# Kernel optimization log

Hardware: AMD Instinct MI355X
Metric: run time of the kernel (lower is better)

## Reference

```python
import jax, jax.numpy as jnp
import numpy as np
import math

B, H, S, D = 2, 8, 2048, 64

def setup_inputs() -> dict:
    key = jax.random.key(0)
    kq, kk, kv, km = jax.random.split(key, 4)
    query = jax.random.uniform(kq, (B, H, S, D), dtype=jnp.float32)
    key_t = jax.random.uniform(kk, (B, H, S, D), dtype=jnp.float32)
    value = jax.random.normal(kv, (B, H, S, D), dtype=jnp.float32)
    mask = jax.random.randint(km, (B, 1, 1, S), 0, 2, dtype=jnp.int32)
    return {"query": query, "key": key_t, "value": value, "mask": mask}

def reference(query, key, value, mask):
    # Non-standard: exp() applied to raw QK^T logits, THEN divided by sqrt(d)
    scores = jnp.exp(jnp.einsum('bhqd,bhkd->bhqk', query, key)) / math.sqrt(query.shape[-1])
    scores = jnp.where(mask == 0, jnp.float32(-1e9), scores)
    p_attn = jax.nn.softmax(scores, axis=-1)
    out = jnp.einsum('bhqk,bhkd->bhqd', p_attn, value)
    return (out, p_attn)
```

## Files before the change

kernel.cpp:

```cpp
#include <hip/hip_runtime.h>
#include <hip/hip_bf16.h>
#include <math.h>

#define NB 2
#define NH 8
#define NS 2048
#define ND 64
#define NBH (NB*NH)
#define QB 128
#define KT 64
#define NTILES (NS/KT)
#define NTHR 512
#define KSTR 72

typedef short bf16x8 __attribute__((ext_vector_type(8)));
typedef short bf16x4 __attribute__((ext_vector_type(4)));
typedef float f32x16 __attribute__((ext_vector_type(16)));

__device__ __forceinline__ short f2bf_trunc(float x){
  unsigned u = __builtin_bit_cast(unsigned, x);
  return (short)(u >> 16);
}
__device__ __forceinline__ float bf2f(short s){
  unsigned u = ((unsigned)(unsigned short)s) << 16;
  return __builtin_bit_cast(float, u);
}
__device__ __forceinline__ short f2bf_rn(float x){
  unsigned u = __builtin_bit_cast(unsigned, x);
  unsigned r = u + 0x7FFFu + ((u >> 16) & 1u);
  return (short)(r >> 16);
}
__device__ __forceinline__ void split3(float x, short &h, short &m, short &lo){
  h = f2bf_trunc(x);  float fh = bf2f(h);
  float r1 = x - fh;  m = f2bf_trunc(r1); float fm = bf2f(m);
  float r2 = r1 - fm; lo = f2bf_trunc(r2);
}

__global__ __launch_bounds__(NTHR, 2)
void attn_mfma_kernel(const float* __restrict__ Qg, const float* __restrict__ Kg,
                      const float* __restrict__ Vg, const int* __restrict__ Mg,
                      float* __restrict__ outO, float* __restrict__ outP)
{
  __shared__ __align__(16) short sKh[KT*KSTR];
  __shared__ __align__(16) short sKm[KT*KSTR];
  __shared__ __align__(16) short sKl[KT*KSTR];
  __shared__ __align__(16) short sVT[ND*KSTR];
  __shared__ __align__(16) short sP[QB*KSTR];
  __shared__ unsigned sMaskW[NS/32];
  __shared__ float sRedM[8*32], sRedS[8*32];

  const int tid = threadIdx.x;
  const int w  = tid >> 6;
  const int l  = tid & 63;
  const int wm = w >> 1;
  const int wn = w & 1;
  const int lc = l & 31;
  const int lh = l >> 5;

  const int bh = blockIdx.x >> 4;
  const int q0 = (blockIdx.x & 15) * QB;
  const int bb = bh >> 3;
  const size_t base = (size_t)bh * NS * ND;

  if (tid < NS/32) {
    unsigned wbits = 0;
    const int* mp = Mg + bb*NS + tid*32;
    #pragma unroll
    for (int i = 0; i < 32; ++i) wbits |= (mp[i] ? (1u << i) : 0u);
    sMaskW[tid] = wbits;
  }

  bf16x8 qh[4], qm[4], ql[4];
  {
    const float* qp = Qg + base + (size_t)(q0 + wm*32 + lc) * ND;
    #pragma unroll
    for (int ks = 0; ks < 4; ++ks) {
      const int d0 = ks*16 + lh*8;
      float4 f0 = *(const float4*)(qp + d0);
      float4 f1 = *(const float4*)(qp + d0 + 4);
      float xs[8] = {f0.x,f0.y,f0.z,f0.w,f1.x,f1.y,f1.z,f1.w};
      #pragma unroll
      for (int j = 0; j < 8; ++j) {
        short h, m, lo; split3(xs[j], h, m, lo);
        qh[ks][j] = h; qm[ks][j] = m; ql[ks][j] = lo;
      }
    }
  }

  const int s_kk = tid >> 3;
  const int s_d8 = (tid & 7) * 8;
  float4 ka, kb;
  auto loadK = [&](int kt){
    const float* kp = Kg + base + (size_t)(kt*KT + s_kk)*ND + s_d8;
    ka = *(const float4*)(kp);
    kb = *(const float4*)(kp + 4);
  };
  auto writeK = [&](){
    float xs[8] = {ka.x,ka.y,ka.z,ka.w,kb.x,kb.y,kb.z,kb.w};
    bf16x8 vh, vm, vl;
    #pragma unroll
    for (int j = 0; j < 8; ++j) {
      short h, m, lo; split3(xs[j], h, m, lo);
      vh[j] = h; vm[j] = m; vl[j] = lo;
    }
    const int off = s_kk*KSTR + s_d8;
    *(bf16x8*)(&sKh[off]) = vh;
    *(bf16x8*)(&sKm[off]) = vm;
    *(bf16x8*)(&sKl[off]) = vl;
  };

  const int v_dd = tid & 63;
  const int v_k4 = (tid >> 6) * 4;
  float va[4], vb[4];
  auto loadV = [&](int kt){
    const float* vp = Vg + base + (size_t)(kt*KT)*ND + v_dd;
    #pragma unroll
    for (int i = 0; i < 4; ++i) {
      va[i] = vp[(v_k4 + i) * ND];
      vb[i] = vp[(v_k4 + 32 + i) * ND];
    }
  };
  auto writeV = [&](){
    const int swz = ((v_dd >> 3) & 7) << 3;
    bf16x4 pa, pb;
    #pragma unroll
    for (int i = 0; i < 4; ++i) { pa[i] = f2bf_rn(va[i]); pb[i] = f2bf_rn(vb[i]); }
    *(bf16x4*)(&sVT[v_dd*KSTR + (v_k4 ^ swz)])        = pa;
    *(bf16x4*)(&sVT[v_dd*KSTR + ((v_k4 + 32) ^ swz)]) = pb;
  };

  auto qk_tile = [&](f32x16 &accA, f32x16 &accB){
    #pragma unroll
    for (int ks = 0; ks < 4; ++ks) {
      const int off = (wn*32 + lc)*KSTR + ks*16 + lh*8;
      bf16x8 b_h = *(const bf16x8*)(&sKh[off]);
      bf16x8 b_m = *(const bf16x8*)(&sKm[off]);
      bf16x8 b_l = *(const bf16x8*)(&sKl[off]);
      accA = __builtin_amdgcn_mfma_f32_32x32x16_bf16(qh[ks], b_h, accA, 0, 0, 0);
      accB = __builtin_amdgcn_mfma_f32_32x32x16_bf16(qh[ks], b_m, accB, 0, 0, 0);
      accB = __builtin_amdgcn_mfma_f32_32x32x16_bf16(qm[ks], b_h, accB, 0, 0, 0);
      accB = __builtin_amdgcn_mfma_f32_32x32x16_bf16(qm[ks], b_m, accB, 0, 0, 0);
      accB = __builtin_amdgcn_mfma_f32_32x32x16_bf16(qh[ks], b_l, accB, 0, 0, 0);
      accB = __builtin_amdgcn_mfma_f32_32x32x16_bf16(ql[ks], b_h, accB, 0, 0, 0);
    }
  };

  float mx[16], sm[16];
  #pragma unroll
  for (int r = 0; r < 16; ++r) { mx[r] = -INFINITY; sm[r] = 0.f; }

  loadK(0);
  #pragma unroll 1
  for (int kt = 0; kt < NTILES; ++kt) {
    writeK();
    __syncthreads();
    if (kt + 1 < NTILES) loadK(kt + 1);

    f32x16 accA, accB;
    #pragma unroll
    for (int r = 0; r < 16; ++r) { accA[r] = 0.f; accB[r] = 0.f; }
    qk_tile(accA, accB);

    const unsigned mbit = (sMaskW[kt*2 + wn] >> lc) & 1u;
    #pragma unroll
    for (int r = 0; r < 16; ++r) {
      float qk = accA[r] + accB[r];
      float s  = mbit ? __expf(qk) * 0.125f : -1e9f;
      float d  = s - mx[r];
      float e  = __expf(-__builtin_fabsf(d));
      bool  gt = d > 0.f;
      sm[r] = gt ? __builtin_fmaf(sm[r], e, 1.f) : (sm[r] + e);
      mx[r] = gt ? s : mx[r];
    }
    __syncthreads();
  }

  loadK(0); loadV(0);

  #pragma unroll
  for (int r = 0; r < 16; ++r) {
    float m0 = mx[r], s0 = sm[r];
    #pragma unroll
    for (int st = 1; st < 32; st <<= 1) {
      float mo = __shfl_xor(m0, st, 64);
      float so = __shfl_xor(s0, st, 64);
      float nm = fmaxf(m0, mo);
      s0 = s0 * __expf(m0 - nm) + so * __expf(mo - nm);
      m0 = nm;
    }
    mx[r] = m0; sm[r] = s0;
  }
  #pragma unroll
  for (int r = 0; r < 16; ++r) {
    const int row_l = 4*lh + (r & 3) + 8*(r >> 2);
    if (lc == 0) { sRedM[w*32 + row_l] = mx[r]; sRedS[w*32 + row_l] = sm[r]; }
  }
  __syncthreads();
  float inv[16];
  #pragma unroll
  for (int r = 0; r < 16; ++r) {
    const int row_l = 4*lh + (r & 3) + 8*(r >> 2);
    float mo = sRedM[(w ^ 1)*32 + row_l];
    float so = sRedS[(w ^ 1)*32 + row_l];
    float nm = fmaxf(mx[r], mo);
    float s0 = sm[r] * __expf(mx[r] - nm) + so * __expf(mo - nm);
    mx[r] = nm; inv[r] = 1.0f / s0;
  }

  f32x16 accPV;
  #pragma unroll
  for (int r = 0; r < 16; ++r) accPV[r] = 0.f;

  #pragma unroll 1
  for (int kt = 0; kt < NTILES; ++kt) {
    writeK(); writeV();
    __syncthreads();
    if (kt + 1 < NTILES) { loadK(kt + 1); loadV(kt + 1); }

    f32x16 accA, accB;
    #pragma unroll
    for (int r = 0; r < 16; ++r) { accA[r] = 0.f; accB[r] = 0.f; }
    qk_tile(accA, accB);

    const unsigned mbit = (sMaskW[kt*2 + wn] >> lc) & 1u;
    float p[16];
    #pragma unroll
    for (int r = 0; r < 16; ++r) {
      float qk = accA[r] + accB[r];
      float s  = mbit ? __expf(qk) * 0.125f : -1e9f;
      p[r] = __expf(s - mx[r]) * inv[r];
    }

    #pragma unroll
    for (int r = 0; r < 16; ++r) {
      const int row_l = 4*lh + (r & 3) + 8*(r >> 2);
      float po = __shfl_xor(p[r], 1, 64);
      if (!(l & 1)) {
        float* pd = outP + ((size_t)bh*NS + q0 + wm*32 + row_l)*NS + kt*KT + wn*32 + lc;
        float2 f2; f2.x = p[r]; f2.y = po;
        *(float2*)pd = f2;
        unsigned pk = (unsigned)(unsigned short)f2bf_rn(p[r])
                    | ((unsigned)(unsigned short)f2bf_rn(po) << 16);
        *(unsigned*)(&sP[(wm*32 + row_l)*KSTR + wn*32 + lc]) = pk;
      }
    }
    __syncthreads();

    #pragma unroll
    for (int ks = 0; ks < 4; ++ks) {
      bf16x8 pa = *(const bf16x8*)(&sP[(wm*32 + lc)*KSTR + ks*16 + lh*8]);
      const int dg  = wn*32 + lc;
      const int swz = ((dg >> 3) & 7) << 3;
      bf16x8 vB = *(const bf16x8*)(&sVT[dg*KSTR + ((ks*16 + lh*8) ^ swz)]);
      accPV = __builtin_amdgcn_mfma_f32_32x32x16_bf16(pa, vB, accPV, 0, 0, 0);
    }
    __syncthreads();
  }

  #pragma unroll
  for (int r = 0; r < 16; ++r) {
    const int row_l = 4*lh + (r & 3) + 8*(r >> 2);
    outO[base + (size_t)(q0 + wm*32 + row_l)*ND + wn*32 + lc] = accPV[r];
  }
}

extern "C" void kernel_launch(void* const* d_in, const int* in_sizes, int n_in,
                              void* d_out, int out_size, void* d_ws, size_t ws_size,
                              hipStream_t stream) {
  const float* Qg = (const float*)d_in[0];
  const float* Kg = (const float*)d_in[1];
  const float* Vg = (const float*)d_in[2];
  const int*   Mg = (const int*)d_in[3];
  float* outO = (float*)d_out;
  float* outP = (float*)d_out + (size_t)NB*NH*NS*ND;

  dim3 grid(NBH * (NS / QB));
  attn_mfma_kernel<<<grid, NTHR, 0, stream>>>(Qg, Kg, Vg, Mg, outO, outP);
}
```

Measured before the change: 406.2 us.

## Double-buffer K/V tiles in LDS, halve query block, add XOR swizzle and setprio

Halves the query block to 64 rows with 256 threads per block, doubling the grid. K and V tiles are double-buffered in LDS with an XOR swizzle in place of padding, which removes one barrier per tile and overlaps writing the next tile with compute on the current one. The P stores become per-lane scalar writes instead of shuffle-paired float2 stores, and MFMA sections are wrapped in s_setprio. The larger LDS footprint and less vectorized P stores may reduce occupancy or store efficiency.

```diff
diff --git a/kernel.cpp b/kernel.cpp
--- a/kernel.cpp
+++ b/kernel.cpp
@@ -1,5 +1,4 @@
 #include <hip/hip_runtime.h>
-#include <hip/hip_bf16.h>
 #include <math.h>
 
 #define NB 2
@@ -7,14 +6,12 @@
 #define NS 2048
 #define ND 64
 #define NBH (NB*NH)
-#define QB 128
+#define QB 64
 #define KT 64
 #define NTILES (NS/KT)
-#define NTHR 512
-#define KSTR 72
+#define NTHR 256
 
 typedef short bf16x8 __attribute__((ext_vector_type(8)));
-typedef short bf16x4 __attribute__((ext_vector_type(4)));
 typedef float f32x16 __attribute__((ext_vector_type(16)));
 
 __device__ __forceinline__ short f2bf_trunc(float x){
@@ -34,6 +31,9 @@
   h = f2bf_trunc(x);  float fh = bf2f(h);
   float r1 = x - fh;  m = f2bf_trunc(r1); float fm = bf2f(m);
   float r2 = r1 - fm; lo = f2bf_trunc(r2);
+}
+__device__ __forceinline__ int swz(int r, int c){
+  return r*64 + ((((c >> 3) ^ (r & 7)) << 3) | (c & 7));
 }
 
 __global__ __launch_bounds__(NTHR, 2)
@@ -41,13 +41,13 @@
                       const float* __restrict__ Vg, const int* __restrict__ Mg,
                       float* __restrict__ outO, float* __restrict__ outP)
 {
-  __shared__ __align__(16) short sKh[KT*KSTR];
-  __shared__ __align__(16) short sKm[KT*KSTR];
-  __shared__ __align__(16) short sKl[KT*KSTR];
-  __shared__ __align__(16) short sVT[ND*KSTR];
-  __shared__ __align__(16) short sP[QB*KSTR];
+  __shared__ __align__(16) short sKh[2][KT*ND];
+  __shared__ __align__(16) short sKm[2][KT*ND];
+  __shared__ __align__(16) short sKl[2][KT*ND];
+  __shared__ __align__(16) short sVT[2][ND*KT];
+  __shared__ __align__(16) short sP[QB*KT];
   __shared__ unsigned sMaskW[NS/32];
-  __shared__ float sRedM[8*32], sRedS[8*32];
+  __shared__ float sRedM[4*32], sRedS[4*32];
 
   const int tid = threadIdx.x;
   const int w  = tid >> 6;
@@ -57,8 +57,8 @@
   const int lc = l & 31;
   const int lh = l >> 5;
 
-  const int bh = blockIdx.x >> 4;
-  const int q0 = (blockIdx.x & 15) * QB;
+  const int bh = blockIdx.x >> 5;
+  const int q0 = (blockIdx.x & 31) * QB;
   const int bb = bh >> 3;
   const size_t base = (size_t)bh * NS * ND;
 
@@ -87,55 +87,58 @@
     }
   }
 
-  const int s_kk = tid >> 3;
-  const int s_d8 = (tid & 7) * 8;
-  float4 ka, kb;
+  const int s_r = tid >> 2;
+  const int s_c = (tid & 3) * 16;
+  float4 kv0, kv1, kv2, kv3;
   auto loadK = [&](int kt){
-    const float* kp = Kg + base + (size_t)(kt*KT + s_kk)*ND + s_d8;
-    ka = *(const float4*)(kp);
-    kb = *(const float4*)(kp + 4);
-  };
-  auto writeK = [&](){
-    float xs[8] = {ka.x,ka.y,ka.z,ka.w,kb.x,kb.y,kb.z,kb.w};
-    bf16x8 vh, vm, vl;
-    #pragma unroll
-    for (int j = 0; j < 8; ++j) {
-      short h, m, lo; split3(xs[j], h, m, lo);
-      vh[j] = h; vm[j] = m; vl[j] = lo;
-    }
-    const int off = s_kk*KSTR + s_d8;
-    *(bf16x8*)(&sKh[off]) = vh;
-    *(bf16x8*)(&sKm[off]) = vm;
-    *(bf16x8*)(&sKl[off]) = vl;
-  };
-
-  const int v_dd = tid & 63;
-  const int v_k4 = (tid >> 6) * 4;
-  float va[4], vb[4];
+    const float* kp = Kg + base + (size_t)(kt*KT + s_r)*ND + s_c;
+    kv0 = ((const float4*)kp)[0]; kv1 = ((const float4*)kp)[1];
+    kv2 = ((const float4*)kp)[2]; kv3 = ((const float4*)kp)[3];
+  };
+  auto writeK = [&](int b){
+    float xs[16] = {kv0.x,kv0.y,kv0.z,kv0.w, kv1.x,kv1.y,kv1.z,kv1.w,
+                    kv2.x,kv2.y,kv2.z,kv2.w, kv3.x,kv3.y,kv3.z,kv3.w};
+    #pragma unroll
+    for (int half = 0; half < 2; ++half) {
+      bf16x8 vh, vm, vl;
+      #pragma unroll
+      for (int j = 0; j < 8; ++j) {
+        short h, m, lo; split3(xs[half*8 + j], h, m, lo);
+        vh[j] = h; vm[j] = m; vl[j] = lo;
+      }
+      const int off = swz(s_r, s_c + half*8);
+      *(bf16x8*)(&sKh[b][off]) = vh;
+      *(bf16x8*)(&sKm[b][off]) = vm;
+      *(bf16x8*)(&sKl[b][off]) = vl;
+    }
+  };
+
+  const int v_d = tid & 63;
+  const int v_k = (tid >> 6) * 16;
+  float vv[16];
   auto loadV = [&](int kt){
-    const float* vp = Vg + base + (size_t)(kt*KT)*ND + v_dd;
-    #pragma unroll
-    for (int i = 0; i < 4; ++i) {
-      va[i] = vp[(v_k4 + i) * ND];
-      vb[i] = vp[(v_k4 + 32 + i) * ND];
-    }
-  };
-  auto writeV = [&](){
-    const int swz = ((v_dd >> 3) & 7) << 3;
-    bf16x4 pa, pb;
-    #pragma unroll
-    for (int i = 0; i < 4; ++i) { pa[i] = f2bf_rn(va[i]); pb[i] = f2bf_rn(vb[i]); }
-    *(bf16x4*)(&sVT[v_dd*KSTR + (v_k4 ^ swz)])        = pa;
-    *(bf16x4*)(&sVT[v_dd*KSTR + ((v_k4 + 32) ^ swz)]) = pb;
-  };
-
-  auto qk_tile = [&](f32x16 &accA, f32x16 &accB){
+    const float* vp = Vg + base + (size_t)(kt*KT + v_k)*ND + v_d;
+    #pragma unroll
+    for (int i = 0; i < 16; ++i) vv[i] = vp[i*ND];
+  };
+  auto writeV = [&](int b){
+    #pragma unroll
+    for (int half = 0; half < 2; ++half) {
+      bf16x8 t;
+      #pragma unroll
+      for (int j = 0; j < 8; ++j) t[j] = f2bf_rn(vv[half*8 + j]);
+      *(bf16x8*)(&sVT[b][swz(v_d, v_k + half*8)]) = t;
+    }
+  };
+
+  auto qk_tile = [&](int b, f32x16 &accA, f32x16 &accB){
+    __builtin_amdgcn_s_setprio(1);
     #pragma unroll
     for (int ks = 0; ks < 4; ++ks) {
-      const int off = (wn*32 + lc)*KSTR + ks*16 + lh*8;
-      bf16x8 b_h = *(const bf16x8*)(&sKh[off]);
-      bf16x8 b_m = *(const bf16x8*)(&sKm[off]);
-      bf16x8 b_l = *(const bf16x8*)(&sKl[off]);
+      const int off = swz(wn*32 + lc, ks*16 + lh*8);
+      bf16x8 b_h = *(const bf16x8*)(&sKh[b][off]);
+      bf16x8 b_m = *(const bf16x8*)(&sKm[b][off]);
+      bf16x8 b_l = *(const bf16x8*)(&sKl[b][off]);
       accA = __builtin_amdgcn_mfma_f32_32x32x16_bf16(qh[ks], b_h, accA, 0, 0, 0);
       accB = __builtin_amdgcn_mfma_f32_32x32x16_bf16(qh[ks], b_m, accB, 0, 0, 0);
       accB = __builtin_amdgcn_mfma_f32_32x32x16_bf16(qm[ks], b_h, accB, 0, 0, 0);
@@ -143,39 +146,43 @@
       accB = __builtin_amdgcn_mfma_f32_32x32x16_bf16(qh[ks], b_l, accB, 0, 0, 0);
       accB = __builtin_amdgcn_mfma_f32_32x32x16_bf16(ql[ks], b_h, accB, 0, 0, 0);
     }
+    __builtin_amdgcn_s_setprio(0);
   };
 
   float mx[16], sm[16];
   #pragma unroll
-  for (int r = 0; r < 16; ++r) { mx[r] = -INFINITY; sm[r] = 0.f; }
-
-  loadK(0);
+  for (int r = 0; r < 16; ++r) { mx[r] = -3.0e38f; sm[r] = 0.f; }
+
+  loadK(0); writeK(0);
+  int cur = 0;
   #pragma unroll 1
   for (int kt = 0; kt < NTILES; ++kt) {
-    writeK();
     __syncthreads();
-    if (kt + 1 < NTILES) loadK(kt + 1);
+    const bool np = (kt + 1 < NTILES);
+    if (np) loadK(kt + 1);
 
     f32x16 accA, accB;
     #pragma unroll
     for (int r = 0; r < 16; ++r) { accA[r] = 0.f; accB[r] = 0.f; }
-    qk_tile(accA, accB);
-
-    const unsigned mbit = (sMaskW[kt*2 + wn] >> lc) & 1u;
+    qk_tile(cur, accA, accB);
+
+    const unsigned mbit_w = sMaskW[kt*2 + wn];
     #pragma unroll
     for (int r = 0; r < 16; ++r) {
       float qk = accA[r] + accB[r];
-      float s  = mbit ? __expf(qk) * 0.125f : -1e9f;
+      float s  = ((mbit_w >> lc) & 1u) ? __expf(qk) * 0.125f : -1e9f;
       float d  = s - mx[r];
       float e  = __expf(-__builtin_fabsf(d));
       bool  gt = d > 0.f;
       sm[r] = gt ? __builtin_fmaf(sm[r], e, 1.f) : (sm[r] + e);
       mx[r] = gt ? s : mx[r];
     }
-    __syncthreads();
+    if (np) writeK(cur ^ 1);
+    cur ^= 1;
   }
 
   loadK(0); loadV(0);
+  writeK(0); writeV(0);
 
   #pragma unroll
   for (int r = 0; r < 16; ++r) {
@@ -211,50 +218,41 @@
   #pragma unroll
   for (int r = 0; r < 16; ++r) accPV[r] = 0.f;
 
+  cur = 0;
   #pragma unroll 1
   for (int kt = 0; kt < NTILES; ++kt) {
-    writeK(); writeV();
     __syncthreads();
-    if (kt + 1 < NTILES) { loadK(kt + 1); loadV(kt + 1); }
+    const bool np = (kt + 1 < NTILES);
+    if (np) { loadK(kt + 1); loadV(kt + 1); }
 
     f32x16 accA, accB;
     #pragma unroll
     for (int r = 0; r < 16; ++r) { accA[r] = 0.f; accB[r] = 0.f; }
-    qk_tile(accA, accB);
-
-    const unsigned mbit = (sMaskW[kt*2 + wn] >> lc) & 1u;
-    float p[16];
+    qk_tile(cur, accA, accB);
+
+    const unsigned mbit_w = sMaskW[kt*2 + wn];
+    float* pOutBase = outP + ((size_t)bh*NS + q0 + wm*32)*NS + kt*KT + wn*32 + lc;
     #pragma unroll
     for (int r = 0; r < 16; ++r) {
       float qk = accA[r] + accB[r];
-      float s  = mbit ? __expf(qk) * 0.125f : -1e9f;
-      p[r] = __expf(s - mx[r]) * inv[r];
-    }
-
-    #pragma unroll
-    for (int r = 0; r < 16; ++r) {
+      float s  = ((mbit_w >> lc) & 1u) ? __expf(qk) * 0.125f : -1e9f;
+      float p  = __expf(s - mx[r]) * inv[r];
       const int row_l = 4*lh + (r & 3) + 8*(r >> 2);
-      float po = __shfl_xor(p[r], 1, 64);
-      if (!(l & 1)) {
-        float* pd = outP + ((size_t)bh*NS + q0 + wm*32 + row_l)*NS + kt*KT + wn*32 + lc;
-        float2 f2; f2.x = p[r]; f2.y = po;
-        *(float2*)pd = f2;
-        unsigned pk = (unsigned)(unsigned short)f2bf_rn(p[r])
-                    | ((unsigned)(unsigned short)f2bf_rn(po) << 16);
-        *(unsigned*)(&sP[(wm*32 + row_l)*KSTR + wn*32 + lc]) = pk;
-      }
-    }
+      pOutBase[(size_t)row_l * NS] = p;
+      sP[swz(wm*32 + row_l, wn*32 + lc)] = f2bf_rn(p);
+    }
+    if (np) { writeK(cur ^ 1); writeV(cur ^ 1); }
     __syncthreads();
 
+    __builtin_amdgcn_s_setprio(1);
     #pragma unroll
     for (int ks = 0; ks < 4; ++ks) {
-      bf16x8 pa = *(const bf16x8*)(&sP[(wm*32 + lc)*KSTR + ks*16 + lh*8]);
-      const int dg  = wn*32 + lc;
-      const int swz = ((dg >> 3) & 7) << 3;
-      bf16x8 vB = *(const bf16x8*)(&sVT[dg*KSTR + ((ks*16 + lh*8) ^ swz)]);
+      bf16x8 pa = *(const bf16x8*)(&sP[swz(wm*32 + lc, ks*16 + lh*8)]);
+      bf16x8 vB = *(const bf16x8*)(&sVT[cur][swz(wn*32 + lc, ks*16 + lh*8)]);
       accPV = __builtin_amdgcn_mfma_f32_32x32x16_bf16(pa, vB, accPV, 0, 0, 0);
     }
-    __syncthreads();
+    __builtin_amdgcn_s_setprio(0);
+    cur ^= 1;
   }
 
   #pragma unroll
```

Measured after the change: 410.8 us. No clear change (+1.1%).
